# Optimization experiments

Hardware: AMD Instinct MI355X
Metric: run time of the kernel (lower is better)

Reference implementation:

```python
import jax, jax.numpy as jnp
import numpy as np

B, S, D = 4, 2048, 1024
MAG_SCALE = 5.0


def setup_inputs() -> dict:
    key = jax.random.key(0)
    ks = jax.random.split(key, 16)
    sd = 1.0 / np.sqrt(D)  # keep pre-activations O(1)
    inp = {
        "x": jax.random.normal(ks[0], (B, S, D), jnp.float32),
        "W_omega": jax.random.normal(ks[1], (D, D), jnp.float32) * sd,
        "b_omega": jnp.zeros((D,), jnp.float32),
        "W_mag": jax.random.normal(ks[2], (D, D), jnp.float32) * sd,
        "b_mag": jnp.zeros((D,), jnp.float32),
        "W_phi0": jax.random.normal(ks[3], (D, D), jnp.float32) * sd,
        "b_phi0": jnp.zeros((D,), jnp.float32),
        "W_gate": jax.random.normal(ks[4], (D, D), jnp.float32) * sd,
        "b_gate": jnp.zeros((D,), jnp.float32),
        "W_q": jax.random.normal(ks[5], (D, D), jnp.float32) * sd,
        "b_q": jnp.zeros((D,), jnp.float32),
        "integration_scale": jax.random.uniform(ks[6], (D,), jnp.float32),
        "W_out": jax.random.normal(ks[7], (4 * D, D), jnp.float32) * (1.0 / np.sqrt(4 * D)),
        "b_out": jnp.zeros((D,), jnp.float32),
    }
    return inp


def reference(x, W_omega, b_omega, W_mag, b_mag, W_phi0, b_phi0,
              W_gate, b_gate, W_q, b_q, integration_scale, W_out, b_out):
    lin = lambda h, W, b: h @ W + b  # [B,S,*] @ [*,Dout]

    omega = lin(x, W_omega, b_omega)                      # phase velocity [B,S,D]
    magnitude = jax.nn.sigmoid(lin(x, W_mag, b_mag)) * MAG_SCALE
    gate = jax.nn.sigmoid(lin(x, W_gate, b_gate))
    gated_omega = gate * (omega * jnp.abs(integration_scale))
    phi = lin(x, W_phi0, b_phi0) + jnp.cumsum(gated_omega, axis=1)  # integrated phase

    cos_phi = jnp.cos(phi)
    sin_phi = jnp.sin(phi)

    # holographic memory write: cumulative complex binding of content with phase
    weighted_content = magnitude * x
    memory_real = jnp.cumsum(weighted_content * cos_phi, axis=1)
    memory_imag = jnp.cumsum(weighted_content * sin_phi, axis=1)
    sqrt_mag = jnp.sqrt(jnp.cumsum(magnitude, axis=1) + 1e-8)
    memory_real = memory_real / sqrt_mag
    memory_imag = memory_imag / sqrt_mag

    # complex retrieval at a query phase
    phi_q = phi + lin(x, W_q, b_q)
    cos_q, sin_q = jnp.cos(phi_q), jnp.sin(phi_q)
    retrieved_real = memory_real * cos_q + memory_imag * sin_q
    retrieved_imag = memory_imag * cos_q - memory_real * sin_q

    context = jnp.concatenate(
        [x * cos_phi, x * sin_phi, retrieved_real, retrieved_imag], axis=-1)  # [B,S,4D]
    return x + lin(context, W_out, b_out)


if __name__ == "__main__":
    out = reference(**setup_inputs())
    print(out.shape, out.dtype)
```

## Files before the change

kernel.cpp:

```cpp
#include <hip/hip_runtime.h>
#include <hip/hip_fp16.h>

#define B_ 4
#define S_ 2048
#define D_ 1024
#define CCH 64
#define LCH 32
#define NELEM ((size_t)B_*S_*D_)
#define MROWS (B_*S_)

typedef __attribute__((ext_vector_type(4))) float f32x4;
typedef __attribute__((ext_vector_type(8))) _Float16 f16x8;

__device__ __forceinline__ ushort f2h(float v) {
  __half h = __float2half(v);
  return __builtin_bit_cast(ushort, h);
}
__device__ __forceinline__ float h2f(ushort u) {
  return __half2float(__builtin_bit_cast(__half, u));
}

__device__ __forceinline__ void gload16(const ushort* src, char* ldsdst) {
  __builtin_amdgcn_global_load_lds(
      (const __attribute__((address_space(1))) void*)src,
      (__attribute__((address_space(3))) void*)ldsdst, 16, 0, 0);
}


__global__ void xhalf_kernel(const float* __restrict__ x, ushort* __restrict__ xh) {
  size_t i = ((size_t)blockIdx.x * blockDim.x + threadIdx.x) * 8;
  if (i >= NELEM) return;
  float4 a = *(const float4*)(x + i);
  float4 b = *(const float4*)(x + i + 4);
  ushort h[8] = {f2h(a.x), f2h(a.y), f2h(a.z), f2h(a.w),
                 f2h(b.x), f2h(b.y), f2h(b.z), f2h(b.w)};
  *(ushort4*)(xh + i) = *(ushort4*)h;
  *(ushort4*)(xh + i + 4) = *(ushort4*)(h + 4);
}

__global__ void transpose5(const float* __restrict__ W0, const float* __restrict__ W1,
                           const float* __restrict__ W2, const float* __restrict__ W3,
                           const float* __restrict__ W4, ushort* __restrict__ Th) {
  __shared__ float tile[64][65];
  const int z = blockIdx.z;
  const float* W = (z == 0) ? W0 : (z == 1) ? W1 : (z == 2) ? W2 : (z == 3) ? W3 : W4;
  ushort* T = Th + (size_t)z * D_ * D_;
  const int k0 = blockIdx.x * 64, n0 = blockIdx.y * 64;
  const int tx = threadIdx.x & 63, ty = threadIdx.x >> 6;
#pragma unroll
  for (int i = 0; i < 16; ++i)
    tile[ty * 16 + i][tx] = W[(size_t)(k0 + ty * 16 + i) * D_ + n0 + tx];
  __syncthreads();
#pragma unroll
  for (int i = 0; i < 16; ++i) {
    const int nn = ty * 16 + i;
    T[(size_t)(n0 + nn) * D_ + k0 + tx] = f2h(tile[tx][nn]);
  }
}

__global__ void transpose_convert(const float* __restrict__ W, ushort* __restrict__ Th, int sh,
                                  int Kd, int Nd) {
  __shared__ float tile[64][65];
  const int k0 = blockIdx.x * 64, n0 = blockIdx.y * 64;
  const int tx = threadIdx.x & 63, ty = threadIdx.x >> 6;
#pragma unroll
  for (int i = 0; i < 16; ++i)
    tile[ty * 16 + i][tx] = W[(size_t)(k0 + ty * 16 + i) * Nd + n0 + tx];
  __syncthreads();
#pragma unroll
  for (int i = 0; i < 16; ++i) {
    const int nn = ty * 16 + i;
    Th[(size_t)(n0 + nn) * sh + k0 + tx] = f2h(tile[tx][nn]);
  }
}

template <int FINAL>
__global__ __launch_bounds__(512, 2) void gemm128(
    const ushort* __restrict__ A, int lda, const ushort* __restrict__ Bw,
    ushort* __restrict__ Ch, ushort* __restrict__ C4h,
    float* __restrict__ Cf, const float* __restrict__ xres, const float* __restrict__ bias,
    int M, int K) {
  __shared__ __align__(16) char ldsc[3 * 24576];
  const int bid = blockIdx.x;
  const int tm = bid & 63, tn = bid >> 6;
  const int ldb = K;
  const int NT = K >> 5;
  const int t = threadIdx.x, lane = t & 63, wid = t >> 6;
  const int wm = wid >> 2, wn = wid & 3;

  f32x4 acc[4][4];
#pragma unroll
  for (int i = 0; i < 4; ++i)
#pragma unroll
    for (int j = 0; j < 4; ++j) acc[i][j] = (f32x4){0.f, 0.f, 0.f, 0.f};

  const int line1 = t >> 3;
  const int g8s = (t & 7) ^ (line1 & 7);
  const int rowS = line1 * 2 + (g8s >> 2);
  const int kgS = (g8s & 3) << 3;
  const ushort* srcA = A + (size_t)(tm * 128 + rowS) * lda + kgS;
  const ushort* srcB = Bw + (size_t)(tn * 256 + rowS) * ldb + kgS;
  char* dstA = ldsc + (size_t)t * 16;
  char* dstB = ldsc + 8192 + (size_t)t * 16;

  auto STAGE = [&](int tile, int slot) {
    const int ts = (tile < NT) ? tile : NT - 1;
    char* ba = dstA + slot * 24576;
    char* bb = dstB + slot * 24576;
    const ushort* sa = srcA + ts * 32;
    const ushort* sb = srcB + ts * 32;
    gload16(sa, ba);
    gload16(sb, bb);
    gload16(sb + (size_t)128 * ldb, bb + 8192);
  };

  const int lane15 = lane & 15;
  const int hl = lane15 >> 1;
  const int swz = ((((lane15 & 1) << 2) + (lane >> 4)) ^ hl) << 4;
  const char* aB = ldsc + wm * 4096 + hl * 128 + swz;
  const char* bB = ldsc + 8192 + wn * 4096 + hl * 128 + swz;

  STAGE(0, 0); STAGE(1, 1);
  asm volatile("s_waitcnt vmcnt(3)" ::: "memory");
  __builtin_amdgcn_sched_barrier(0);
  __builtin_amdgcn_s_barrier();

  int s_rd = 0, s_st = 2;
#pragma unroll 1
  for (int tt = 0; tt < NT; ++tt) {
    STAGE(tt + 2, s_st);
    const char* ab = aB + s_rd * 24576;
    const char* bb = bB + s_rd * 24576;
    f16x8 af[4], bf_[4];
#pragma unroll
    for (int f = 0; f < 4; ++f) af[f] = *(const f16x8*)(ab + f * 1024);
#pragma unroll
    for (int c = 0; c < 4; ++c) bf_[c] = *(const f16x8*)(bb + c * 1024);
    asm volatile("s_waitcnt lgkmcnt(0)" ::: "memory");
    __builtin_amdgcn_sched_barrier(0);
    __builtin_amdgcn_s_setprio(1);
#pragma unroll
    for (int f = 0; f < 4; ++f)
#pragma unroll
      for (int c = 0; c < 4; ++c)
        acc[f][c] = __builtin_amdgcn_mfma_f32_16x16x32_f16(af[f], bf_[c], acc[f][c], 0, 0, 0);
    __builtin_amdgcn_s_setprio(0);
    asm volatile("s_waitcnt vmcnt(3)" ::: "memory");
    __builtin_amdgcn_sched_barrier(0);
    __builtin_amdgcn_s_barrier();
    s_rd = (s_rd == 2) ? 0 : s_rd + 1;
    s_st = (s_st == 2) ? 0 : s_st + 1;
  }

#pragma unroll
  for (int i = 0; i < 4; ++i) {
    const int row0 = tm * 128 + wm * 64 + i * 16 + ((lane >> 4) << 2);
#pragma unroll
    for (int jj = 0; jj < 4; ++jj) {
      const int col = tn * 256 + wn * 64 + jj * 16 + lane15;
      if (FINAL) {
#pragma unroll
        for (int r = 0; r < 4; ++r) {
          const size_t idx = (size_t)(row0 + r) * 1024 + col;
          Cf[idx] = acc[i][jj][r] + xres[idx] + bias[col];
        }
      } else {
        const int pl = col >> 10;
        ushort* base = (pl < 4) ? (Ch + (size_t)pl * (size_t)M * 1024) : C4h;
#pragma unroll
        for (int r = 0; r < 4; ++r)
          base[(size_t)(row0 + r) * 1024 + (col & 1023)] = f2h(acc[i][jj][r]);
      }
    }
  }
}


__device__ __forceinline__ void load4h(const ushort* p, float* f) {
  ushort4 u = *(const ushort4*)p;
  f[0] = h2f(u.x); f[1] = h2f(u.y); f[2] = h2f(u.z); f[3] = h2f(u.w);
}

__global__ void prep_chunk_kernel(ushort* __restrict__ omega_go, const ushort* __restrict__ gate_lin,
                                  ushort* __restrict__ mag_io,
                                  const float* __restrict__ b_om, const float* __restrict__ b_gate,
                                  const float* __restrict__ b_mag, const float* __restrict__ isc,
                                  float* __restrict__ gsum, float* __restrict__ msum) {
  int tid = blockIdx.x * blockDim.x + threadIdx.x;
  if (tid >= B_ * CCH * (D_ / 4)) return;
  int d4 = tid & 255, c = (tid >> 8) & (CCH - 1), b = tid >> 14;
  int d = d4 * 4;
  size_t base = ((size_t)(b * S_) + c * LCH) * D_ + d;
  size_t cs = ((size_t)(b * CCH) + c) * D_ + d;
  float bo[4], bg[4], bm[4], is[4];
  *(float4*)bo = *(const float4*)(b_om + d);
  *(float4*)bg = *(const float4*)(b_gate + d);
  *(float4*)bm = *(const float4*)(b_mag + d);
  *(float4*)is = *(const float4*)(isc + d);
  float sg[4] = {0.f, 0.f, 0.f, 0.f}, sm[4] = {0.f, 0.f, 0.f, 0.f};
  for (int s = 0; s < LCH; ++s) {
    size_t i = base + (size_t)s * D_;
    float om[4], gl[4], mg[4];
    load4h(omega_go + i, om);
    load4h(gate_lin + i, gl);
    load4h(mag_io + i, mg);
    ushort wo[4], wm_[4];
#pragma unroll
    for (int j = 0; j < 4; ++j) {
      float g = 1.f / (1.f + __expf(-(gl[j] + bg[j])));
      float m5 = 5.f / (1.f + __expf(-(mg[j] + bm[j])));
      float go = g * ((om[j] + bo[j]) * fabsf(is[j]));
      sg[j] += go;
      sm[j] += m5;
      wo[j] = f2h(go);
      wm_[j] = f2h(m5);
    }
    *(ushort4*)(omega_go + i) = *(ushort4*)wo;
    *(ushort4*)(mag_io + i) = *(ushort4*)wm_;
  }
  *(float4*)(gsum + cs) = *(float4*)sg;
  *(float4*)(msum + cs) = *(float4*)sm;
}

__global__ void scan_offsets_kernel(float* __restrict__ s1, float* __restrict__ s2) {
  int gw = (blockIdx.x * blockDim.x + threadIdx.x) >> 6;
  int lane = threadIdx.x & 63;
  if (gw >= B_ * D_) return;
  int d = gw & (D_ - 1), b = gw >> 10;
  size_t idx = ((size_t)(b * CCH) + lane) * D_ + d;
  float v1 = s1[idx], v2 = s2[idx];
#pragma unroll
  for (int off = 1; off < 64; off <<= 1) {
    float u1 = __shfl_up(v1, off);
    float u2 = __shfl_up(v2, off);
    if (lane >= off) { v1 += u1; v2 += u2; }
  }
  float e1 = __shfl_up(v1, 1), e2 = __shfl_up(v2, 1);
  if (lane == 0) { e1 = 0.f; e2 = 0.f; }
  s1[idx] = e1;
  s2[idx] = e2;
}

__global__ void phase_scan_kernel(const ushort* __restrict__ xh, const ushort* __restrict__ go,
                                  const ushort* __restrict__ mag, const ushort* __restrict__ p0,
                                  const float* __restrict__ goff,
                                  float* __restrict__ trsum, float* __restrict__ tisum,
                                  const float* __restrict__ b_phi, ushort* __restrict__ ctx) {
  int tid = blockIdx.x * blockDim.x + threadIdx.x;
  if (tid >= B_ * CCH * (D_ / 4)) return;
  int d4 = tid & 255, c = (tid >> 8) & (CCH - 1), b = tid >> 14;
  int d = d4 * 4;
  size_t base = ((size_t)(b * S_) + c * LCH) * D_ + d;
  size_t cs = ((size_t)(b * CCH) + c) * D_ + d;
  float pr[4], bp[4];
  *(float4*)pr = *(const float4*)(goff + cs);
  *(float4*)bp = *(const float4*)(b_phi + d);
  float tr[4] = {0.f, 0.f, 0.f, 0.f}, ti[4] = {0.f, 0.f, 0.f, 0.f};
  size_t crow = ((size_t)(b * S_ + c * LCH)) * 4096 + d;
  for (int s = 0; s < LCH; ++s) {
    size_t i = base + (size_t)s * D_;
    float g[4], ph0[4], m[4], xv[4];
    load4h(go + i, g);
    load4h(p0 + i, ph0);
    load4h(mag + i, m);
    load4h(xh + i, xv);
    ushort c4[4], s4[4];
#pragma unroll
    for (int j = 0; j < 4; ++j) {
      pr[j] += g[j];
      float ph = ph0[j] + bp[j] + pr[j];
      float sp, cp;
      __sincosf(ph, &sp, &cp);
      float wr = m[j] * xv[j];
      tr[j] += wr * cp;
      ti[j] += wr * sp;
      c4[j] = f2h(xv[j] * cp);
      s4[j] = f2h(xv[j] * sp);
    }
    *(ushort4*)(ctx + crow) = *(ushort4*)c4;
    *(ushort4*)(ctx + crow + 1024) = *(ushort4*)s4;
    crow += 4096;
  }
  *(float4*)(trsum + cs) = *(float4*)tr;
  *(float4*)(tisum + cs) = *(float4*)ti;
}

__global__ void retrieve_kernel(const ushort* __restrict__ xh, const ushort* __restrict__ go,
                                const ushort* __restrict__ mag, const ushort* __restrict__ p0,
                                const ushort* __restrict__ q,
                                const float* __restrict__ goff, const float* __restrict__ moff,
                                const float* __restrict__ troff, const float* __restrict__ tioff,
                                const float* __restrict__ b_phi, const float* __restrict__ b_q,
                                ushort* __restrict__ ctx) {
  int tid = blockIdx.x * blockDim.x + threadIdx.x;
  if (tid >= B_ * CCH * (D_ / 4)) return;
  int d4 = tid & 255, c = (tid >> 8) & (CCH - 1), b = tid >> 14;
  int d = d4 * 4;
  size_t base = ((size_t)(b * S_) + c * LCH) * D_ + d;
  size_t cs = ((size_t)(b * CCH) + c) * D_ + d;
  float pr[4], mr[4], tr[4], ti[4], bp[4], bq[4];
  *(float4*)pr = *(const float4*)(goff + cs);
  *(float4*)mr = *(const float4*)(moff + cs);
  *(float4*)tr = *(const float4*)(troff + cs);
  *(float4*)ti = *(const float4*)(tioff + cs);
  *(float4*)bp = *(const float4*)(b_phi + d);
  *(float4*)bq = *(const float4*)(b_q + d);
  size_t crow = ((size_t)(b * S_ + c * LCH)) * 4096 + d;
  for (int s = 0; s < LCH; ++s) {
    size_t i = base + (size_t)s * D_;
    float g[4], ph0[4], m[4], xv[4], qv[4];
    load4h(go + i, g);
    load4h(p0 + i, ph0);
    load4h(mag + i, m);
    load4h(q + i, qv);
    load4h(xh + i, xv);
    ushort r2[4], r3[4];
#pragma unroll
    for (int j = 0; j < 4; ++j) {
      pr[j] += g[j];
      float ph = ph0[j] + bp[j] + pr[j];
      float sp, cp;
      __sincosf(ph, &sp, &cp);
      mr[j] += m[j];
      float wr = m[j] * xv[j];
      tr[j] += wr * cp;
      ti[j] += wr * sp;
      float rs = rsqrtf(mr[j] + 1e-8f);
      float mreal = tr[j] * rs, mimag = ti[j] * rs;
      float phq = ph + qv[j] + bq[j];
      float sq, cq;
      __sincosf(phq, &sq, &cq);
      r2[j] = f2h(mreal * cq + mimag * sq);
      r3[j] = f2h(mimag * cq - mreal * sq);
    }
    *(ushort4*)(ctx + crow + 2048) = *(ushort4*)r2;
    *(ushort4*)(ctx + crow + 3072) = *(ushort4*)r3;
    crow += 4096;
  }
}

extern "C" void kernel_launch(void* const* d_in, const int* in_sizes, int n_in,
                              void* d_out, int out_size, void* d_ws, size_t ws_size,
                              hipStream_t stream) {
  const float* x      = (const float*)d_in[0];
  const float* W_om   = (const float*)d_in[1];
  const float* b_om   = (const float*)d_in[2];
  const float* W_mag  = (const float*)d_in[3];
  const float* b_mag  = (const float*)d_in[4];
  const float* W_phi  = (const float*)d_in[5];
  const float* b_phi  = (const float*)d_in[6];
  const float* W_gate = (const float*)d_in[7];
  const float* b_gate = (const float*)d_in[8];
  const float* W_q    = (const float*)d_in[9];
  const float* b_q    = (const float*)d_in[10];
  const float* isc    = (const float*)d_in[11];
  const float* W_out  = (const float*)d_in[12];
  const float* b_out  = (const float*)d_in[13];
  float* out = (float*)d_out;

  const size_t WS_NEEDED = 213909504ull;
  if (ws_size < WS_NEEDED) {
    (void)hipMemsetAsync(d_out, 0, (size_t)out_size * sizeof(float), stream);
    return;
  }
  char* w = (char*)d_ws;
  ushort* planes_h = (ushort*)w;
  ushort* omega_buf = planes_h;
  ushort* gate_buf  = planes_h + NELEM;
  ushort* mag_buf   = planes_h + 2 * NELEM;
  ushort* phi0_buf  = planes_h + 3 * NELEM;
  ushort* x_h   = (ushort*)(w + 67108864);
  ushort* q_buf = (ushort*)out;
  char* ctxb = w + 4 * NELEM * 4;
  ushort* ctx   = (ushort*)ctxb;
  ushort* W5T   = (ushort*)(ctxb + 16777216);
  ushort* WoutT = (ushort*)(w + 201326592);
  float* gsum  = (float*)(w + 209715200);
  float* msum  = (float*)(w + 210763776);
  float* trsum = (float*)(w + 211812352);
  float* tisum = (float*)(w + 212860928);

  xhalf_kernel<<<(int)(NELEM / 2048), 256, 0, stream>>>(x, x_h);
  transpose5<<<dim3(16, 16, 5), 256, 0, stream>>>(W_om, W_gate, W_mag, W_phi, W_q, W5T);
  transpose_convert<<<dim3(64, 16), 256, 0, stream>>>(W_out, WoutT, 4096, 4 * D_, D_);

  gemm128<0><<<1280, 512, 0, stream>>>(x_h, 1024, W5T, planes_h, q_buf,
                                       nullptr, nullptr, nullptr, MROWS, 1024);

  prep_chunk_kernel<<<B_ * CCH * (D_ / 4) / 256, 256, 0, stream>>>(
      omega_buf, gate_buf, mag_buf, b_om, b_gate, b_mag, isc, gsum, msum);
  scan_offsets_kernel<<<B_ * D_ * 64 / 256, 256, 0, stream>>>(gsum, msum);
  phase_scan_kernel<<<B_ * CCH * (D_ / 4) / 256, 256, 0, stream>>>(
      x_h, omega_buf, mag_buf, phi0_buf, gsum, trsum, tisum, b_phi, ctx);
  scan_offsets_kernel<<<B_ * D_ * 64 / 256, 256, 0, stream>>>(trsum, tisum);
  retrieve_kernel<<<B_ * CCH * (D_ / 4) / 256, 256, 0, stream>>>(
      x_h, omega_buf, mag_buf, phi0_buf, q_buf, gsum, msum, trsum, tisum, b_phi, b_q, ctx);

  gemm128<1><<<256, 512, 0, stream>>>(ctx, 4096, WoutT, nullptr, nullptr, out,
                                      x, b_out, MROWS, 4 * D_);
}
```

Baseline: 291.1 us.

## Templatize GEMM tile width and use double-buffered LDS pipeline

Generalizes the GEMM over the N-tile width and launches the output projection with 128-wide tiles and twice as many blocks, to better fill the GPU's compute units. It also replaces the three-stage LDS prefetch ring with a two-stage double buffer that waits for all outstanding loads each iteration. This trades reduced latency hiding in both GEMMs for lower LDS use and more parallelism in the final GEMM.

New measurement: 304.3 us. 1.05x slower.

```diff
diff --git a/kernel.cpp b/kernel.cpp
--- a/kernel.cpp
+++ b/kernel.cpp
@@ -74,13 +74,15 @@
   }
 }
 
-template <int FINAL>
-__global__ __launch_bounds__(512, 2) void gemm128(
+template <int FINAL, int BN>
+__global__ __launch_bounds__(512, 2) void gemmT(
     const ushort* __restrict__ A, int lda, const ushort* __restrict__ Bw,
     ushort* __restrict__ Ch, ushort* __restrict__ C4h,
     float* __restrict__ Cf, const float* __restrict__ xres, const float* __restrict__ bias,
     int M, int K) {
-  __shared__ __align__(16) char ldsc[3 * 24576];
+  constexpr int SLICE = 8192 + BN * 64;
+  constexpr int JJ = BN / 64;
+  __shared__ __align__(16) char ldsc[2 * SLICE];
   const int bid = blockIdx.x;
   const int tm = bid & 63, tn = bid >> 6;
   const int ldb = K;
@@ -88,76 +90,71 @@
   const int t = threadIdx.x, lane = t & 63, wid = t >> 6;
   const int wm = wid >> 2, wn = wid & 3;
 
-  f32x4 acc[4][4];
+  f32x4 acc[4][JJ];
 #pragma unroll
   for (int i = 0; i < 4; ++i)
 #pragma unroll
-    for (int j = 0; j < 4; ++j) acc[i][j] = (f32x4){0.f, 0.f, 0.f, 0.f};
+    for (int j = 0; j < JJ; ++j) acc[i][j] = (f32x4){0.f, 0.f, 0.f, 0.f};
 
   const int line1 = t >> 3;
   const int g8s = (t & 7) ^ (line1 & 7);
   const int rowS = line1 * 2 + (g8s >> 2);
   const int kgS = (g8s & 3) << 3;
   const ushort* srcA = A + (size_t)(tm * 128 + rowS) * lda + kgS;
-  const ushort* srcB = Bw + (size_t)(tn * 256 + rowS) * ldb + kgS;
+  const ushort* srcB = Bw + (size_t)(tn * BN + rowS) * ldb + kgS;
   char* dstA = ldsc + (size_t)t * 16;
   char* dstB = ldsc + 8192 + (size_t)t * 16;
 
   auto STAGE = [&](int tile, int slot) {
     const int ts = (tile < NT) ? tile : NT - 1;
-    char* ba = dstA + slot * 24576;
-    char* bb = dstB + slot * 24576;
-    const ushort* sa = srcA + ts * 32;
-    const ushort* sb = srcB + ts * 32;
-    gload16(sa, ba);
-    gload16(sb, bb);
-    gload16(sb + (size_t)128 * ldb, bb + 8192);
+    char* ba = dstA + slot * SLICE;
+    char* bb = dstB + slot * SLICE;
+    gload16(srcA + ts * 32, ba);
+    gload16(srcB + ts * 32, bb);
+    if (BN == 256) gload16(srcB + (size_t)128 * ldb + ts * 32, bb + 8192);
   };
 
   const int lane15 = lane & 15;
   const int hl = lane15 >> 1;
   const int swz = ((((lane15 & 1) << 2) + (lane >> 4)) ^ hl) << 4;
   const char* aB = ldsc + wm * 4096 + hl * 128 + swz;
-  const char* bB = ldsc + 8192 + wn * 4096 + hl * 128 + swz;
-
-  STAGE(0, 0); STAGE(1, 1);
-  asm volatile("s_waitcnt vmcnt(3)" ::: "memory");
+  const char* bB = ldsc + 8192 + wn * ((BN / 4) * 64) + hl * 128 + swz;
+
+  STAGE(0, 0);
+  asm volatile("s_waitcnt vmcnt(0)" ::: "memory");
   __builtin_amdgcn_sched_barrier(0);
   __builtin_amdgcn_s_barrier();
 
-  int s_rd = 0, s_st = 2;
 #pragma unroll 1
   for (int tt = 0; tt < NT; ++tt) {
-    STAGE(tt + 2, s_st);
-    const char* ab = aB + s_rd * 24576;
-    const char* bb = bB + s_rd * 24576;
-    f16x8 af[4], bf_[4];
+    STAGE(tt + 1, (tt + 1) & 1);
+    const char* ab = aB + (tt & 1) * SLICE;
+    const char* bb = bB + (tt & 1) * SLICE;
+    f16x8 af[4], bf_[JJ];
 #pragma unroll
     for (int f = 0; f < 4; ++f) af[f] = *(const f16x8*)(ab + f * 1024);
 #pragma unroll
-    for (int c = 0; c < 4; ++c) bf_[c] = *(const f16x8*)(bb + c * 1024);
+    for (int c = 0; c < JJ; ++c) bf_[c] = *(const f16x8*)(bb + c * 1024);
     asm volatile("s_waitcnt lgkmcnt(0)" ::: "memory");
     __builtin_amdgcn_sched_barrier(0);
     __builtin_amdgcn_s_setprio(1);
 #pragma unroll
     for (int f = 0; f < 4; ++f)
 #pragma unroll
-      for (int c = 0; c < 4; ++c)
+      for (int c = 0; c < JJ; ++c)
         acc[f][c] = __builtin_amdgcn_mfma_f32_16x16x32_f16(af[f], bf_[c], acc[f][c], 0, 0, 0);
     __builtin_amdgcn_s_setprio(0);
-    asm volatile("s_waitcnt vmcnt(3)" ::: "memory");
+    asm volatile("s_waitcnt vmcnt(0)" ::: "memory");
     __builtin_amdgcn_sched_barrier(0);
     __builtin_amdgcn_s_barrier();
-    s_rd = (s_rd == 2) ? 0 : s_rd + 1;
-    s_st = (s_st == 2) ? 0 : s_st + 1;
   }
 
 #pragma unroll
   for (int i = 0; i < 4; ++i) {
     const int row0 = tm * 128 + wm * 64 + i * 16 + ((lane >> 4) << 2);
 #pragma unroll
-    for (int jj = 0; jj < 4; ++jj) {
-      const int col = tn * 256 + wn * 64 + jj * 16 + lane15;
+    for (int jj = 0; jj < JJ; ++jj) {
+      const int col = tn * BN + wn * (BN / 4) + jj * 16 + lane15;
       if (FINAL) {
 #pragma unroll
         for (int r = 0; r < 4; ++r) {
@@ -384,8 +381,8 @@
   transpose5<<<dim3(16, 16, 5), 256, 0, stream>>>(W_om, W_gate, W_mag, W_phi, W_q, W5T);
   transpose_convert<<<dim3(64, 16), 256, 0, stream>>>(W_out, WoutT, 4096, 4 * D_, D_);
 
-  gemm128<0><<<1280, 512, 0, stream>>>(x_h, 1024, W5T, planes_h, q_buf,
-                                       nullptr, nullptr, nullptr, MROWS, 1024);
+  gemmT<0, 256><<<1280, 512, 0, stream>>>(x_h, 1024, W5T, planes_h, q_buf,
+                                          nullptr, nullptr, nullptr, MROWS, 1024);
 
   prep_chunk_kernel<<<B_ * CCH * (D_ / 4) / 256, 256, 0, stream>>>(
       omega_buf, gate_buf, mag_buf, b_om, b_gate, b_mag, isc, gsum, msum);
@@ -396,6 +393,6 @@
   retrieve_kernel<<<B_ * CCH * (D_ / 4) / 256, 256, 0, stream>>>(
       x_h, omega_buf, mag_buf, phi0_buf, q_buf, gsum, msum, trsum, tisum, b_phi, b_q, ctx);
 
-  gemm128<1><<<256, 512, 0, stream>>>(ctx, 4096, WoutT, nullptr, nullptr, out,
-                                      x, b_out, MROWS, 4 * D_);
-}
+  gemmT<1, 128><<<512, 512, 0, stream>>>(ctx, 4096, WoutT, nullptr, nullptr, out,
+                                         x, b_out, MROWS, 4 * D_);
+}
```
